# Optimization experiments

Measured on AMD Instinct MI355X. Metric: run time of the kernel, lower is better.

The kernel has to match this reference:

```python
import jax, jax.numpy as jnp
import numpy as np

N_NODES = 100000
N_EDGES = 1200000
MAX_ATOM_TYPE = 100
NUM_FEATURES = 92
GC_DIM = 64          # pre_layer_dim == gc_dim == CGConv channels
NUM_RBF = 32
NUM_GC_LAYERS = 4
CUTOFF_UPPER = 5.0
BN_EPS = 1e-5


def setup_inputs() -> dict:
    key = jax.random.key(0)
    ks = jax.random.split(key, 12)
    atom_types = jax.random.randint(ks[0], (N_NODES,), 0, MAX_ATOM_TYPE, dtype=jnp.int32)
    pos = jax.random.uniform(ks[1], (N_NODES, 3), dtype=jnp.float32) * 6.0  # box side 6 -> many dists < cutoff
    edge_index = jax.random.randint(ks[2], (2, N_EDGES), 0, N_NODES, dtype=jnp.int32)
    # parameters
    emb = jax.random.normal(ks[3], (MAX_ATOM_TYPE, NUM_FEATURES), dtype=jnp.float32)
    s = 1.0 / np.sqrt(NUM_FEATURES)
    pre_W = jax.random.uniform(ks[4], (NUM_FEATURES, GC_DIM), minval=-s, maxval=s, dtype=jnp.float32)
    pre_b = jnp.zeros((GC_DIM,), jnp.float32)
    zdim = 2 * GC_DIM + NUM_RBF  # [x_i, x_j, edge_attr]
    sz = 1.0 / np.sqrt(zdim)
    Wf = jax.random.uniform(ks[5], (NUM_GC_LAYERS, zdim, GC_DIM), minval=-sz, maxval=sz, dtype=jnp.float32)
    bf = jnp.zeros((NUM_GC_LAYERS, GC_DIM), jnp.float32)
    Ws = jax.random.uniform(ks[6], (NUM_GC_LAYERS, zdim, GC_DIM), minval=-sz, maxval=sz, dtype=jnp.float32)
    bs = jnp.zeros((NUM_GC_LAYERS, GC_DIM), jnp.float32)
    bn_gamma = jnp.ones((NUM_GC_LAYERS, GC_DIM), jnp.float32)
    bn_beta = jnp.zeros((NUM_GC_LAYERS, GC_DIM), jnp.float32)
    # ExpNormalSmearing (torchmd-net) init
    start = np.exp(-CUTOFF_UPPER)
    means = jnp.asarray(np.linspace(start, 1.0, NUM_RBF), jnp.float32)
    betas = jnp.full((NUM_RBF,), (2.0 / NUM_RBF * (1.0 - start)) ** -2, jnp.float32)
    return {"atom_types": atom_types, "pos": pos, "edge_index": edge_index,
            "emb": emb, "pre_W": pre_W, "pre_b": pre_b,
            "Wf": Wf, "bf": bf, "Ws": Ws, "bs": bs,
            "bn_gamma": bn_gamma, "bn_beta": bn_beta,
            "means": means, "betas": betas}


def _forward(atom_types, pos, edge_index, emb, pre_W, pre_b, Wf, bf, Ws, bs,
             bn_gamma, bn_beta, means, betas):
    src, dst = edge_index[0], edge_index[1]
    # distance (edge_vec = pos[src] - pos[dst])
    vec = pos[src] - pos[dst]                                  # [E,3]
    dist = jnp.sqrt(jnp.sum(vec * vec, axis=-1) + 1e-12)       # [E]
    # expnorm RBF with cosine cutoff (cutoff_lower = 0)
    cutoff = 0.5 * (jnp.cos(dist * (np.pi / CUTOFF_UPPER)) + 1.0) * (dist < CUTOFF_UPPER)
    alpha = 5.0 / CUTOFF_UPPER
    edge_attr = cutoff[:, None] * jnp.exp(
        -betas * (jnp.exp(-alpha * dist)[:, None] - means) ** 2)  # [E,NUM_RBF]
    # embedding + pre layer
    x = emb[atom_types]                                        # [N,F]
    x = jax.nn.relu(x @ pre_W + pre_b)                         # [N,C]
    # mean-aggregation degree (scatter-mean denominator)
    deg = jax.ops.segment_sum(jnp.ones_like(dist), dst, num_segments=N_NODES)
    inv_deg = jnp.where(deg > 0, 1.0 / jnp.maximum(deg, 1.0), 0.0)[:, None]
    for l in range(NUM_GC_LAYERS):
        # CGConv: z = [x_i, x_j, e]; out = x + mean_j(sigmoid(lin_f(z)) * softplus(lin_s(z)))
        z = jnp.concatenate([x[dst], x[src], edge_attr], axis=-1)   # [E, 2C+R]
        msg = jax.nn.sigmoid(z @ Wf[l] + bf[l]) * jax.nn.softplus(z @ Ws[l] + bs[l])
        agg = jax.ops.segment_sum(msg, dst, num_segments=N_NODES) * inv_deg
        x = x + agg
        # BatchNorm1d (batch statistics, biased var, as in torch training mode)
        mu = jnp.mean(x, axis=0)
        var = jnp.mean((x - mu) ** 2, axis=0)
        x = (x - mu) * jax.lax.rsqrt(var + BN_EPS) * bn_gamma[l] + bn_beta[l]
    return x


def reference(atom_types, pos, edge_index, emb, pre_W, pre_b, Wf, bf, Ws, bs,
              bn_gamma, bn_beta, means, betas):
    return _forward(atom_types, pos, edge_index, emb, pre_W, pre_b, Wf, bf, Ws, bs,
                    bn_gamma, bn_beta, means, betas)
```

## Files before the change

kernel.cpp:

```cpp
#include <hip/hip_runtime.h>
#include <math.h>

#define N_NODES 100000
#define N_EDGES 1200000
#define GC 64
#define RBF 32
#define NLAYERS 4
#define NF 92
#define NATOM 100
#define BN_EPS 1e-5f
#define TILE_GRID 2048
#define NWIN (N_EDGES / 16)
#define LOG2E 1.44269504f
#define LN2 0.69314718f

typedef _Float16 half8 __attribute__((ext_vector_type(8)));
typedef _Float16 half4 __attribute__((ext_vector_type(4)));
typedef _Float16 half2v __attribute__((ext_vector_type(2)));
typedef float f32x4 __attribute__((ext_vector_type(4)));
union U32H2 { unsigned int u; half2v h; };

__global__ __launch_bounds__(256) void deg_kernel(
    const int* __restrict__ ei, int* __restrict__ deg)
{
    int e = blockIdx.x * 256 + threadIdx.x;
    if (e >= N_EDGES) return;
    atomicAdd(&deg[ei[N_EDGES + e]], 1);
}

__global__ __launch_bounds__(256) void scan_a_kernel(const int* __restrict__ deg, int* __restrict__ bsums)
{
    __shared__ int sm[256];
    int tid = threadIdx.x;
    int i = blockIdx.x * 256 + tid;
    int v = (i < N_NODES) ? deg[i] : 0;
    sm[tid] = v;
    __syncthreads();
    for (int s = 128; s > 0; s >>= 1) {
        if (tid < s) sm[tid] += sm[tid + s];
        __syncthreads();
    }
    if (tid == 0) bsums[blockIdx.x] = sm[0];
}

__global__ __launch_bounds__(512) void scan_b_kernel(const int* __restrict__ bsums, int* __restrict__ boffs)
{
    __shared__ int sm[512];
    int tid = threadIdx.x;
    int v = (tid < 391) ? bsums[tid] : 0;
    sm[tid] = v;
    __syncthreads();
    for (int off = 1; off < 512; off <<= 1) {
        int t = (tid >= off) ? sm[tid - off] : 0;
        __syncthreads();
        sm[tid] += t;
        __syncthreads();
    }
    boffs[tid] = (tid == 0) ? 0 : sm[tid - 1];
}

__global__ __launch_bounds__(256) void scan_c_kernel(
    const int* __restrict__ deg, const int* __restrict__ boffs,
    int* __restrict__ row_st, float* __restrict__ inv_deg)
{
    __shared__ int sm[256];
    int tid = threadIdx.x;
    int i = blockIdx.x * 256 + tid;
    int v = (i < N_NODES) ? deg[i] : 0;
    sm[tid] = v;
    __syncthreads();
    for (int off = 1; off < 256; off <<= 1) {
        int t = (tid >= off) ? sm[tid - off] : 0;
        __syncthreads();
        sm[tid] += t;
        __syncthreads();
    }
    if (i <= N_NODES) row_st[i] = boffs[blockIdx.x] + sm[tid] - v;
    if (i < N_NODES) inv_deg[i] = (v > 0) ? (1.0f / (float)v) : 0.0f;
}

__global__ __launch_bounds__(256) void scatter_perm_kernel(
    const int* __restrict__ ei, const int* __restrict__ row_st,
    int* __restrict__ cursor, int2* __restrict__ csr_sd)
{
    int e = blockIdx.x * 256 + threadIdx.x;
    if (e >= N_EDGES) return;
    int s = ei[e];
    int d = ei[N_EDGES + e];
    int p = atomicAdd(&cursor[d], 1);
    csr_sd[row_st[d] + p] = make_int2(s, d);
}

__global__ __launch_bounds__(256) void split_kernel(
    const int2* __restrict__ csr_sd, int* __restrict__ csr_src, int* __restrict__ csr_dst)
{
    int i = blockIdx.x * 256 + threadIdx.x;
    if (i >= N_EDGES) return;
    int2 v = csr_sd[i];
    csr_src[i] = v.x;
    csr_dst[i] = v.y;
}

__global__ __launch_bounds__(256) void rbf_kernel(
    const int* __restrict__ csr_src, const int* __restrict__ csr_dst,
    const float* __restrict__ pos,
    const float* __restrict__ means, const float* __restrict__ betas,
    unsigned int* __restrict__ ea)
{
    int idx = blockIdx.x * 256 + threadIdx.x;
    if (idx >= N_EDGES) return;
    int s = csr_src[idx];
    int d = csr_dst[idx];
    float dx = pos[s * 3 + 0] - pos[d * 3 + 0];
    float dy = pos[s * 3 + 1] - pos[d * 3 + 1];
    float dz = pos[s * 3 + 2] - pos[d * 3 + 2];
    float dist = sqrtf(dx * dx + dy * dy + dz * dz + 1e-12f);

    float cut = 0.0f;
    if (dist < 5.0f) cut = 0.5f * (__cosf(dist * 0.6283185307179586f) + 1.0f);
    float ex = __expf(-dist);
    union { _Float16 h[32]; uint4 u[4]; } pk;
#pragma unroll
    for (int k = 0; k < 32; k++) {
        float v = ex - means[k];
        pk.h[k] = (_Float16)(cut * __expf(-betas[k] * v * v));
    }
    uint4* op = (uint4*)(ea + (size_t)idx * 16);
    op[0] = pk.u[0];
    op[1] = pk.u[1];
    op[2] = pk.u[2];
    op[3] = pk.u[3];
}

__global__ __launch_bounds__(256) void window_prep_kernel(
    const int* __restrict__ csr_dst, const float* __restrict__ inv_deg,
    unsigned char* __restrict__ seg8, int* __restrict__ wnode, _Float16* __restrict__ inv_e)
{
    int w = blockIdx.x * 256 + threadIdx.x;
    if (w >= NWIN) return;
    int base = w * 16;
    int prev = -1, s = -1;
    for (int k = 0; k < 16; k++) {
        int d = csr_dst[base + k];
        if (d != prev) { s++; prev = d; wnode[base + s] = d; }
        seg8[base + k] = (unsigned char)s;
        inv_e[base + k] = (_Float16)(inv_deg[d] * LN2);
    }
    for (int m = s + 1; m < 16; m++) wnode[base + m] = -1;
}

__global__ __launch_bounds__(256) void wcvt_kernel(
    const float* __restrict__ Wf, const float* __restrict__ Ws,
    _Float16* __restrict__ wf16, _Float16* __restrict__ ws16)
{
    int i = blockIdx.x * 256 + threadIdx.x;
    int l = i / (160 * GC);
    int r = i - l * 160 * GC;
    int k = r >> 6;
    int col = r & 63;
    size_t o = ((size_t)l * GC + col) * 160 + k;
    wf16[o] = (_Float16)(Wf[i] * LOG2E);
    ws16[o] = (_Float16)(Ws[i] * LOG2E);
}

__global__ __launch_bounds__(64) void atom_table_kernel(
    const float* __restrict__ emb, const float* __restrict__ pre_W,
    const float* __restrict__ pre_b, float* __restrict__ T)
{
    int a = blockIdx.x;
    int c = threadIdx.x;
    float acc = pre_b[c];
    for (int k = 0; k < NF; k++) acc = fmaf(emb[a * NF + k], pre_W[k * GC + c], acc);
    T[a * GC + c] = fmaxf(acc, 0.0f);
}

__global__ __launch_bounds__(256) void xinit_kernel(
    const int* __restrict__ atom_types, const float* __restrict__ T,
    float* __restrict__ x, _Float16* __restrict__ x16)
{
    int i = blockIdx.x * 256 + threadIdx.x;
    int n = i >> 4;
    int a = atom_types[n];
    float4 v = ((const float4*)T)[a * 16 + (i & 15)];
    ((float4*)x)[i] = v;
    half4 h = { (_Float16)v.x, (_Float16)v.y, (_Float16)v.z, (_Float16)v.w };
    ((half4*)x16)[i] = h;
}

static __device__ __forceinline__ void proj_mfma16(
    const _Float16* __restrict__ wf, const _Float16* __restrict__ ws,
    const float* __restrict__ bfv, const float* __restrict__ bsv,
    const half8 Bn[2], int cb, int node, unsigned int* __restrict__ P2u)
{
    const int lane = threadIdx.x & 63;
    const int quad = lane >> 4;
    const int r16 = lane & 15;
    f32x4 accf[2], accs[2];
#pragma unroll
    for (int sub = 0; sub < 2; sub++) {
        accf[sub] = (f32x4){0.f, 0.f, 0.f, 0.f};
        accs[sub] = (f32x4){0.f, 0.f, 0.f, 0.f};
    }
#pragma unroll
    for (int kt = 0; kt < 2; kt++) {
#pragma unroll
        for (int sub = 0; sub < 2; sub++) {
            int chan = cb + sub * 16 + r16;
            half8 a = *(const half8*)(wf + (size_t)chan * 160 + kt * 32 + quad * 8);
            half8 b = *(const half8*)(ws + (size_t)chan * 160 + kt * 32 + quad * 8);
            accf[sub] = __builtin_amdgcn_mfma_f32_16x16x32_f16(a, Bn[kt], accf[sub], 0, 0, 0);
            accs[sub] = __builtin_amdgcn_mfma_f32_16x16x32_f16(b, Bn[kt], accs[sub], 0, 0, 0);
        }
    }
#pragma unroll
    for (int sub = 0; sub < 2; sub++) {
        float4 bf4 = *(const float4*)(bfv + cb + sub * 16 + quad * 4);
        float4 bs4 = *(const float4*)(bsv + cb + sub * 16 + quad * 4);
        half8 h = { (_Float16)(accf[sub][0] + bf4.x * LOG2E), (_Float16)(accs[sub][0] + bs4.x * LOG2E),
                    (_Float16)(accf[sub][1] + bf4.y * LOG2E), (_Float16)(accs[sub][1] + bs4.y * LOG2E),
                    (_Float16)(accf[sub][2] + bf4.z * LOG2E), (_Float16)(accs[sub][2] + bs4.z * LOG2E),
                    (_Float16)(accf[sub][3] + bf4.w * LOG2E), (_Float16)(accs[sub][3] + bs4.w * LOG2E) };
        *(half8*)(P2u + (size_t)node * GC + cb + sub * 16 + quad * 4) = h;
    }
}

__global__ __launch_bounds__(256) void proj_kernel(
    const _Float16* __restrict__ x16,
    const _Float16* __restrict__ wf, const _Float16* __restrict__ ws,
    const float* __restrict__ bfv, const float* __restrict__ bsv,
    unsigned int* __restrict__ P2u)
{
    const int lane = threadIdx.x & 63;
    const int wid = threadIdx.x >> 6;
    const int quad = lane >> 4;
    const int r16 = lane & 15;
    const int wgid = blockIdx.x * 4 + wid;
    const int cb = (wgid & 1) * 32;
    const int nb = (wgid >> 1) * 16;
    half8 Bn[2];
    Bn[0] = *(const half8*)(x16 + (size_t)(nb + r16) * GC + quad * 8);
    Bn[1] = *(const half8*)(x16 + (size_t)(nb + r16) * GC + 32 + quad * 8);
    proj_mfma16(wf, ws, bfv, bsv, Bn, cb, nb + r16, P2u);
}

__global__ __launch_bounds__(256) void bnproj_kernel(
    const float* __restrict__ xn, const float* __restrict__ stats,
    const float* __restrict__ gamma, const float* __restrict__ beta,
    float* __restrict__ xout, _Float16* __restrict__ x16,
    const _Float16* __restrict__ wf, const _Float16* __restrict__ ws,
    const float* __restrict__ bfv, const float* __restrict__ bsv,
    unsigned int* __restrict__ P2u)
{
    __shared__ _Float16 lx[32 * 72];
    const int nb = blockIdx.x * 32;
    const float invN = 1.0f / (float)N_NODES;

#pragma unroll
    for (int rep = 0; rep < 2; rep++) {
        int g = rep * 256 + threadIdx.x;
        int gi = blockIdx.x * 512 + g;
        int node = g >> 4;
        int c4 = (g & 15) * 4;
        float4 v = ((const float4*)xn)[gi];
        float vv[4] = {v.x, v.y, v.z, v.w};
        float o[4];
#pragma unroll
        for (int t = 0; t < 4; t++) {
            int c = c4 + t;
            float mu = stats[c] * invN;
            float var = stats[64 + c] * invN - mu * mu;
            float sc = gamma[c] * rsqrtf(var + BN_EPS);
            o[t] = (vv[t] - mu) * sc + beta[c];
        }
        ((float4*)xout)[gi] = make_float4(o[0], o[1], o[2], o[3]);
        half4 h = { (_Float16)o[0], (_Float16)o[1], (_Float16)o[2], (_Float16)o[3] };
        ((half4*)x16)[gi] = h;
        *(half4*)(lx + node * 72 + c4) = h;
    }
    __syncthreads();

    const int lane = threadIdx.x & 63;
    const int wid = threadIdx.x >> 6;
    const int quad = lane >> 4;
    const int r16 = lane & 15;
    const int cb = (wid & 1) * 32;
    const int tn = (wid >> 1) * 16 + r16;
    half8 Bn[2];
    Bn[0] = *(const half8*)(lx + tn * 72 + quad * 8);
    Bn[1] = *(const half8*)(lx + tn * 72 + 32 + quad * 8);
    proj_mfma16(wf, ws, bfv, bsv, Bn, cb, nb + tn, P2u);
}

static __device__ __forceinline__ void compute_win(
    half8 S0, half8 S1, half8 E, int4 d4, int moff,
    const half8 (&WGF)[3][2], const half8 (&WGS)[3][2],
    int r16, int quad, int cb,
    const unsigned char* __restrict__ seg8, const int* __restrict__ wnode,
    const _Float16* __restrict__ inv_e, const unsigned int* __restrict__ P2u,
    float* __restrict__ x)
{
    unsigned int pv0, pv1, pv2, pv3, pv4, pv5, pv6, pv7;
    {
        const unsigned int* p0 = P2u + (size_t)d4.x * GC + cb + r16;
        const unsigned int* p1 = P2u + (size_t)d4.y * GC + cb + r16;
        const unsigned int* p2 = P2u + (size_t)d4.z * GC + cb + r16;
        const unsigned int* p3 = P2u + (size_t)d4.w * GC + cb + r16;
        pv0 = p0[0];  pv4 = p0[16];
        pv1 = p1[0];  pv5 = p1[16];
        pv2 = p2[0];  pv6 = p2[16];
        pv3 = p3[0];  pv7 = p3[16];
    }
    unsigned int segq = *(const unsigned int*)(seg8 + moff + quad * 4);
    int4 wn4 = *(const int4*)(wnode + moff + quad * 4);
    half4 inv4 = *(const half4*)(inv_e + moff + quad * 4);

    const f32x4 zf = (f32x4){0.0f, 0.0f, 0.0f, 0.0f};
    f32x4 accf[2], accs[2];
    __builtin_amdgcn_s_setprio(1);
#pragma unroll
    for (int ctl = 0; ctl < 2; ctl++) {
        accf[ctl] = __builtin_amdgcn_mfma_f32_16x16x32_f16(S0, WGF[0][ctl], zf, 0, 0, 0);
        accs[ctl] = __builtin_amdgcn_mfma_f32_16x16x32_f16(S0, WGS[0][ctl], zf, 0, 0, 0);
        accf[ctl] = __builtin_amdgcn_mfma_f32_16x16x32_f16(S1, WGF[1][ctl], accf[ctl], 0, 0, 0);
        accs[ctl] = __builtin_amdgcn_mfma_f32_16x16x32_f16(S1, WGS[1][ctl], accs[ctl], 0, 0, 0);
        accf[ctl] = __builtin_amdgcn_mfma_f32_16x16x32_f16(E,  WGF[2][ctl], accf[ctl], 0, 0, 0);
        accs[ctl] = __builtin_amdgcn_mfma_f32_16x16x32_f16(E,  WGS[2][ctl], accs[ctl], 0, 0, 0);
    }
    __builtin_amdgcn_s_setprio(0);

    unsigned int pvv[8] = {pv0, pv1, pv2, pv3, pv4, pv5, pv6, pv7};
    half4 msgh[2];
#pragma unroll
    for (int ctl = 0; ctl < 2; ctl++) {
#pragma unroll
        for (int rr = 0; rr < 4; rr++) {
            U32H2 t; t.u = pvv[ctl * 4 + rr];
            float af = accf[ctl][rr] + (float)t.h.x;
            float as = accs[ctl][rr] + (float)t.h.y;
            float sg = __builtin_amdgcn_rcpf(1.0f + __builtin_amdgcn_exp2f(-af));
            float sp = __builtin_amdgcn_logf(1.0f + __builtin_amdgcn_exp2f(as));
            msgh[ctl][rr] = (_Float16)(sg * sp);
        }
    }
    half4 am;
#pragma unroll
    for (int j = 0; j < 4; j++) {
        int sj = (segq >> (8 * j)) & 0xff;
        am[j] = (sj == r16) ? inv4[j] : (_Float16)0.0f;
    }
    int wa[4] = { wn4.x, wn4.y, wn4.z, wn4.w };
#pragma unroll
    for (int ctl = 0; ctl < 2; ctl++) {
        f32x4 red = __builtin_amdgcn_mfma_f32_16x16x16f16(am, msgh[ctl], zf, 0, 0, 0);
#pragma unroll
        for (int rr = 0; rr < 4; rr++) {
            int nd = wa[rr];
            if (nd >= 0) atomicAdd(&x[(size_t)nd * GC + cb + ctl * 16 + r16], red[rr]);
        }
    }
}

#define LOADSET(S0_, S1_, EE_, SRC_, WW_)                                            \
    S0_ = *(const half8*)(x16 + (size_t)(SRC_) * GC + quad * 8);                     \
    S1_ = *(const half8*)(x16 + (size_t)(SRC_) * GC + 32 + quad * 8);                \
    EE_ = *(const half8*)(ea + ((size_t)(WW_) * 16 + r16) * RBF + quad * 8);

__global__ __launch_bounds__(256, 4) void win_mfma_kernel(
    const _Float16* __restrict__ x16, const _Float16* __restrict__ ea,
    const int* __restrict__ csr_src, const int* __restrict__ csr_dst,
    const unsigned char* __restrict__ seg8, const int* __restrict__ wnode,
    const _Float16* __restrict__ inv_e, const unsigned int* __restrict__ P2u,
    const _Float16* __restrict__ wf16, const _Float16* __restrict__ ws16,
    float* __restrict__ x)
{
    const int lane = threadIdx.x & 63;
    const int wid = __builtin_amdgcn_readfirstlane(threadIdx.x >> 6);
    const int quad = lane >> 4;
    const int r16 = lane & 15;
    const int wgid = blockIdx.x * 4 + wid;
    const int cb = (wgid & 1) * 32;
    int w = wgid >> 1;
    const int NSEQ = TILE_GRID * 2;

    half8 WGF[3][2], WGS[3][2];
#pragma unroll
    for (int ctl = 0; ctl < 2; ctl++) {
        const _Float16* wfp = wf16 + (size_t)(cb + ctl * 16 + r16) * 160 + 64 + quad * 8;
        const _Float16* wsp = ws16 + (size_t)(cb + ctl * 16 + r16) * 160 + 64 + quad * 8;
#pragma unroll
        for (int kt = 0; kt < 3; kt++) {
            WGF[kt][ctl] = *(const half8*)(wfp + kt * 32);
            WGS[kt][ctl] = *(const half8*)(wsp + kt * 32);
        }
    }

    int sA = csr_src[w * 16 + r16];
    int4 d4A = *(const int4*)(csr_dst + w * 16 + quad * 4);
    half8 AS0, AS1, AE;
    LOADSET(AS0, AS1, AE, sA, w);
    int moffA = w * 16;

    int wB = w + NSEQ; if (wB >= NWIN) wB = NWIN - 1;
    int sB = csr_src[wB * 16 + r16];
    int4 d4B = *(const int4*)(csr_dst + wB * 16 + quad * 4);
    half8 BS0, BS1, BE;
    LOADSET(BS0, BS1, BE, sB, wB);
    int moffB = wB * 16;

    int wC = wB + NSEQ; if (wC >= NWIN) wC = NWIN - 1;
    int sC = csr_src[wC * 16 + r16];
    int4 d4C = *(const int4*)(csr_dst + wC * 16 + quad * 4);

    while (true) {
        compute_win(AS0, AS1, AE, d4A, moffA,
                    WGF, WGS, r16, quad, cb, seg8, wnode, inv_e, P2u, x);
        LOADSET(AS0, AS1, AE, sC, wC);
        d4A = d4C; moffA = wC * 16;
        wC += NSEQ; if (wC >= NWIN) wC = NWIN - 1;
        sC = csr_src[wC * 16 + r16];
        d4C = *(const int4*)(csr_dst + wC * 16 + quad * 4);
        w += NSEQ;
        if (w >= NWIN) break;

        compute_win(BS0, BS1, BE, d4B, moffB,
                    WGF, WGS, r16, quad, cb, seg8, wnode, inv_e, P2u, x);
        LOADSET(BS0, BS1, BE, sC, wC);
        d4B = d4C; moffB = wC * 16;
        wC += NSEQ; if (wC >= NWIN) wC = NWIN - 1;
        sC = csr_src[wC * 16 + r16];
        d4C = *(const int4*)(csr_dst + wC * 16 + quad * 4);
        w += NSEQ;
        if (w >= NWIN) break;
    }
}

__global__ __launch_bounds__(256) void stats_kernel(const float* __restrict__ x, float* __restrict__ stats)
{
    const int lane = threadIdx.x & 63;
    const int wid = threadIdx.x >> 6;
    int w = blockIdx.x * 4 + wid;
    float s1 = 0.0f, s2 = 0.0f;
    for (int n = w; n < N_NODES; n += 1024) {
        float v = x[(size_t)n * GC + lane];
        s1 += v;
        s2 = fmaf(v, v, s2);
    }
    __shared__ float rs1[4][64];
    __shared__ float rs2[4][64];
    rs1[wid][lane] = s1;
    rs2[wid][lane] = s2;
    __syncthreads();
    if (threadIdx.x < 64) {
        atomicAdd(&stats[lane], rs1[0][lane] + rs1[1][lane] + rs1[2][lane] + rs1[3][lane]);
    } else if (threadIdx.x < 128) {
        int c = threadIdx.x & 63;
        atomicAdd(&stats[64 + c], rs2[0][c] + rs2[1][c] + rs2[2][c] + rs2[3][c]);
    }
}

__global__ __launch_bounds__(256) void bn_kernel(
    const float* __restrict__ xn, const float* __restrict__ stats,
    const float* __restrict__ gamma, const float* __restrict__ beta,
    float* __restrict__ out)
{
    int i = blockIdx.x * 256 + threadIdx.x;
    int c4 = (i & 15) * 4;
    float4 v = ((const float4*)xn)[i];
    float vv[4] = {v.x, v.y, v.z, v.w};
    float o[4];
    const float invN = 1.0f / (float)N_NODES;
#pragma unroll
    for (int t = 0; t < 4; t++) {
        int c = c4 + t;
        float mu = stats[c] * invN;
        float var = stats[64 + c] * invN - mu * mu;
        float sc = gamma[c] * rsqrtf(var + BN_EPS);
        o[t] = (vv[t] - mu) * sc + beta[c];
    }
    ((float4*)out)[i] = make_float4(o[0], o[1], o[2], o[3]);
}

extern "C" void kernel_launch(void* const* d_in, const int* in_sizes, int n_in,
                              void* d_out, int out_size, void* d_ws, size_t ws_size,
                              hipStream_t stream)
{
    const int* atom_types = (const int*)d_in[0];
    const float* pos = (const float*)d_in[1];
    const int* edge_index = (const int*)d_in[2];
    const float* emb = (const float*)d_in[3];
    const float* pre_W = (const float*)d_in[4];
    const float* pre_b = (const float*)d_in[5];
    const float* Wf = (const float*)d_in[6];
    const float* bf = (const float*)d_in[7];
    const float* Ws = (const float*)d_in[8];
    const float* bs = (const float*)d_in[9];
    const float* gamma = (const float*)d_in[10];
    const float* beta = (const float*)d_in[11];
    const float* means = (const float*)d_in[12];
    const float* betas = (const float*)d_in[13];

    char* base = (char*)d_ws;
    char* p = base;
    auto alloc = [&](size_t bytes) -> char* {
        char* r = p;
        p += (bytes + 255) & ~(size_t)255;
        return r;
    };
    unsigned int* ea = (unsigned int*)alloc((size_t)N_EDGES * RBF * 2);
    float* x = (float*)alloc((size_t)N_NODES * GC * 4);
    _Float16* x16 = (_Float16*)alloc((size_t)N_NODES * GC * 2);
    unsigned int* P2u = (unsigned int*)alloc((size_t)N_NODES * GC * 4);
    int* csr_src = (int*)alloc((size_t)N_EDGES * 4);
    int* csr_dst = (int*)alloc((size_t)N_EDGES * 4);
    int* wnode = (int*)alloc((size_t)N_EDGES * 4);
    unsigned char* seg8 = (unsigned char*)alloc((size_t)N_EDGES);
    _Float16* inv_e = (_Float16*)alloc((size_t)N_EDGES * 2);
    _Float16* wf16 = (_Float16*)alloc((size_t)NLAYERS * GC * 160 * 2);
    _Float16* ws16 = (_Float16*)alloc((size_t)NLAYERS * GC * 160 * 2);
    int* row_st = (int*)alloc((size_t)(N_NODES + 1) * 4);
    float* inv_deg = (float*)alloc((size_t)N_NODES * 4);
    float* T = (float*)alloc((size_t)NATOM * GC * 4);
    int* bsums = (int*)alloc(512 * 4);
    int* boffs = (int*)alloc(512 * 4);
    const size_t ZR_INTS = (size_t)2 * N_NODES + 128 * NLAYERS + 64;
    char* zr = alloc(ZR_INTS * 4);
    int* deg = (int*)zr;
    int* cursor = deg + N_NODES;
    float* stats = (float*)(cursor + N_NODES);

    int2* csr_sd = (int2*)ea;

    if ((size_t)(p - base) > ws_size) return;

    (void)hipMemsetAsync(zr, 0, ZR_INTS * 4, stream);

    const int EG = (N_EDGES + 255) / 256;
    deg_kernel<<<EG, 256, 0, stream>>>(edge_index, deg);
    scan_a_kernel<<<391, 256, 0, stream>>>(deg, bsums);
    scan_b_kernel<<<1, 512, 0, stream>>>(bsums, boffs);
    scan_c_kernel<<<391, 256, 0, stream>>>(deg, boffs, row_st, inv_deg);
    scatter_perm_kernel<<<EG, 256, 0, stream>>>(edge_index, row_st, cursor, csr_sd);
    split_kernel<<<EG, 256, 0, stream>>>(csr_sd, csr_src, csr_dst);
    rbf_kernel<<<EG, 256, 0, stream>>>(csr_src, csr_dst, pos, means, betas, ea);
    window_prep_kernel<<<(NWIN + 255) / 256, 256, 0, stream>>>(csr_dst, inv_deg, seg8, wnode, inv_e);
    wcvt_kernel<<<(NLAYERS * 160 * GC) / 256, 256, 0, stream>>>(Wf, Ws, wf16, ws16);
    atom_table_kernel<<<NATOM, 64, 0, stream>>>(emb, pre_W, pre_b, T);
    xinit_kernel<<<N_NODES * 16 / 256, 256, 0, stream>>>(atom_types, T, x, x16);
    proj_kernel<<<N_NODES / 32, 256, 0, stream>>>(x16, wf16, ws16, bf, bs, P2u);

    for (int l = 0; l < NLAYERS; l++) {
        win_mfma_kernel<<<TILE_GRID, 256, 0, stream>>>(
            x16, (const _Float16*)ea, csr_src, csr_dst, seg8, wnode, inv_e, P2u,
            wf16 + (size_t)l * GC * 160, ws16 + (size_t)l * GC * 160, x);
        stats_kernel<<<256, 256, 0, stream>>>(x, stats + l * 128);
        if (l < NLAYERS - 1) {
            bnproj_kernel<<<N_NODES / 32, 256, 0, stream>>>(
                x, stats + l * 128, gamma + l * GC, beta + l * GC, x, x16,
                wf16 + (size_t)(l + 1) * GC * 160, ws16 + (size_t)(l + 1) * GC * 160,
                bf + (l + 1) * GC, bs + (l + 1) * GC, P2u);
        } else {
            bn_kernel<<<N_NODES * 16 / 256, 256, 0, stream>>>(
                x, stats + l * 128, gamma + l * GC, beta + l * GC, (float*)d_out);
        }
    }
}
```

Measured before the change: 891.2 us.

## Fuse edge preprocessing kernels, merge constant prep, retune occupancy and stats grid

Combines split, RBF and window-prep into one edge_post kernel that reads the sorted (src,dst) pairs once and builds the window segment data from shared memory. Weight conversion and the atom table go into a single launch, which cuts the number of kernel launches. csr_sd now gets its own buffer instead of aliasing ea, which costs extra workspace. The main kernel's launch bounds drop from 4 to 3 blocks per SM, and the stats kernel grid doubles to 512 blocks with the matching stride change.

```diff
diff --git a/kernel.cpp b/kernel.cpp
--- a/kernel.cpp
+++ b/kernel.cpp
@@ -91,87 +91,86 @@
     csr_sd[row_st[d] + p] = make_int2(s, d);
 }
 
-__global__ __launch_bounds__(256) void split_kernel(
-    const int2* __restrict__ csr_sd, int* __restrict__ csr_src, int* __restrict__ csr_dst)
-{
-    int i = blockIdx.x * 256 + threadIdx.x;
-    if (i >= N_EDGES) return;
-    int2 v = csr_sd[i];
-    csr_src[i] = v.x;
-    csr_dst[i] = v.y;
-}
-
-__global__ __launch_bounds__(256) void rbf_kernel(
-    const int* __restrict__ csr_src, const int* __restrict__ csr_dst,
-    const float* __restrict__ pos,
+__global__ __launch_bounds__(256) void edge_post_kernel(
+    const int2* __restrict__ csr_sd, const float* __restrict__ pos,
+    const float* __restrict__ inv_deg,
     const float* __restrict__ means, const float* __restrict__ betas,
-    unsigned int* __restrict__ ea)
-{
-    int idx = blockIdx.x * 256 + threadIdx.x;
-    if (idx >= N_EDGES) return;
-    int s = csr_src[idx];
-    int d = csr_dst[idx];
-    float dx = pos[s * 3 + 0] - pos[d * 3 + 0];
-    float dy = pos[s * 3 + 1] - pos[d * 3 + 1];
-    float dz = pos[s * 3 + 2] - pos[d * 3 + 2];
-    float dist = sqrtf(dx * dx + dy * dy + dz * dz + 1e-12f);
-
-    float cut = 0.0f;
-    if (dist < 5.0f) cut = 0.5f * (__cosf(dist * 0.6283185307179586f) + 1.0f);
-    float ex = __expf(-dist);
-    union { _Float16 h[32]; uint4 u[4]; } pk;
-#pragma unroll
-    for (int k = 0; k < 32; k++) {
-        float v = ex - means[k];
-        pk.h[k] = (_Float16)(cut * __expf(-betas[k] * v * v));
-    }
-    uint4* op = (uint4*)(ea + (size_t)idx * 16);
-    op[0] = pk.u[0];
-    op[1] = pk.u[1];
-    op[2] = pk.u[2];
-    op[3] = pk.u[3];
-}
-
-__global__ __launch_bounds__(256) void window_prep_kernel(
-    const int* __restrict__ csr_dst, const float* __restrict__ inv_deg,
-    unsigned char* __restrict__ seg8, int* __restrict__ wnode, _Float16* __restrict__ inv_e)
-{
-    int w = blockIdx.x * 256 + threadIdx.x;
-    if (w >= NWIN) return;
-    int base = w * 16;
-    int prev = -1, s = -1;
-    for (int k = 0; k < 16; k++) {
-        int d = csr_dst[base + k];
-        if (d != prev) { s++; prev = d; wnode[base + s] = d; }
-        seg8[base + k] = (unsigned char)s;
-        inv_e[base + k] = (_Float16)(inv_deg[d] * LN2);
-    }
-    for (int m = s + 1; m < 16; m++) wnode[base + m] = -1;
-}
-
-__global__ __launch_bounds__(256) void wcvt_kernel(
+    int* __restrict__ csr_src, int* __restrict__ csr_dst,
+    unsigned int* __restrict__ ea,
+    unsigned char* __restrict__ seg8, int* __restrict__ wnode,
+    _Float16* __restrict__ inv_e)
+{
+    __shared__ int sdst[256];
+    int t = blockIdx.x * 256 + threadIdx.x;
+    if (t < N_EDGES) {
+        int2 v = csr_sd[t];
+        int s = v.x, d = v.y;
+        csr_src[t] = s;
+        csr_dst[t] = d;
+        sdst[threadIdx.x] = d;
+        inv_e[t] = (_Float16)(inv_deg[d] * LN2);
+
+        float dx = pos[s * 3 + 0] - pos[d * 3 + 0];
+        float dy = pos[s * 3 + 1] - pos[d * 3 + 1];
+        float dz = pos[s * 3 + 2] - pos[d * 3 + 2];
+        float dist = sqrtf(dx * dx + dy * dy + dz * dz + 1e-12f);
+        float cut = 0.0f;
+        if (dist < 5.0f) cut = 0.5f * (__cosf(dist * 0.6283185307179586f) + 1.0f);
+        float ex = __expf(-dist);
+        union { _Float16 h[32]; uint4 u[4]; } pk;
+#pragma unroll
+        for (int k = 0; k < 32; k++) {
+            float vk = ex - means[k];
+            pk.h[k] = (_Float16)(cut * __expf(-betas[k] * vk * vk));
+        }
+        uint4* op = (uint4*)(ea + (size_t)t * 16);
+        op[0] = pk.u[0];
+        op[1] = pk.u[1];
+        op[2] = pk.u[2];
+        op[3] = pk.u[3];
+    }
+    __syncthreads();
+    if (threadIdx.x < 16) {
+        int w0 = blockIdx.x * 16 + threadIdx.x;
+        if ((size_t)w0 * 16 < N_EDGES) {
+            int lb = threadIdx.x * 16;
+            int gb = w0 * 16;
+            int prev = -1, sg = -1;
+            for (int k = 0; k < 16; k++) {
+                int dd = sdst[lb + k];
+                if (dd != prev) { sg++; prev = dd; wnode[gb + sg] = dd; }
+                seg8[gb + k] = (unsigned char)sg;
+            }
+            for (int m = sg + 1; m < 16; m++) wnode[gb + m] = -1;
+        }
+    }
+}
+
+__global__ __launch_bounds__(256) void prep_const_kernel(
     const float* __restrict__ Wf, const float* __restrict__ Ws,
-    _Float16* __restrict__ wf16, _Float16* __restrict__ ws16)
-{
-    int i = blockIdx.x * 256 + threadIdx.x;
-    int l = i / (160 * GC);
-    int r = i - l * 160 * GC;
-    int k = r >> 6;
-    int col = r & 63;
-    size_t o = ((size_t)l * GC + col) * 160 + k;
-    wf16[o] = (_Float16)(Wf[i] * LOG2E);
-    ws16[o] = (_Float16)(Ws[i] * LOG2E);
-}
-
-__global__ __launch_bounds__(64) void atom_table_kernel(
+    _Float16* __restrict__ wf16, _Float16* __restrict__ ws16,
     const float* __restrict__ emb, const float* __restrict__ pre_W,
     const float* __restrict__ pre_b, float* __restrict__ T)
 {
-    int a = blockIdx.x;
-    int c = threadIdx.x;
-    float acc = pre_b[c];
-    for (int k = 0; k < NF; k++) acc = fmaf(emb[a * NF + k], pre_W[k * GC + c], acc);
-    T[a * GC + c] = fmaxf(acc, 0.0f);
+    int b = blockIdx.x;
+    if (b < 160) {
+        int i = b * 256 + threadIdx.x;
+        int l = i / (160 * GC);
+        int r = i - l * 160 * GC;
+        int k = r >> 6;
+        int col = r & 63;
+        size_t o = ((size_t)l * GC + col) * 160 + k;
+        wf16[o] = (_Float16)(Wf[i] * LOG2E);
+        ws16[o] = (_Float16)(Ws[i] * LOG2E);
+    } else {
+        int a = (b - 160) * 4 + (threadIdx.x >> 6);
+        int c = threadIdx.x & 63;
+        if (a < NATOM) {
+            float acc = pre_b[c];
+            for (int k = 0; k < NF; k++) acc = fmaf(emb[a * NF + k], pre_W[k * GC + c], acc);
+            T[a * GC + c] = fmaxf(acc, 0.0f);
+        }
+    }
 }
 
 __global__ __launch_bounds__(256) void xinit_kernel(
@@ -365,7 +364,7 @@
     S1_ = *(const half8*)(x16 + (size_t)(SRC_) * GC + 32 + quad * 8);                \
     EE_ = *(const half8*)(ea + ((size_t)(WW_) * 16 + r16) * RBF + quad * 8);
 
-__global__ __launch_bounds__(256, 4) void win_mfma_kernel(
+__global__ __launch_bounds__(256, 3) void win_mfma_kernel(
     const _Float16* __restrict__ x16, const _Float16* __restrict__ ea,
     const int* __restrict__ csr_src, const int* __restrict__ csr_dst,
     const unsigned char* __restrict__ seg8, const int* __restrict__ wnode,
@@ -440,7 +439,7 @@
     const int wid = threadIdx.x >> 6;
     int w = blockIdx.x * 4 + wid;
     float s1 = 0.0f, s2 = 0.0f;
-    for (int n = w; n < N_NODES; n += 1024) {
+    for (int n = w; n < N_NODES; n += 2048) {
         float v = x[(size_t)n * GC + lane];
         s1 += v;
         s2 = fmaf(v, v, s2);
@@ -510,6 +509,7 @@
     float* x = (float*)alloc((size_t)N_NODES * GC * 4);
     _Float16* x16 = (_Float16*)alloc((size_t)N_NODES * GC * 2);
     unsigned int* P2u = (unsigned int*)alloc((size_t)N_NODES * GC * 4);
+    int2* csr_sd = (int2*)alloc((size_t)N_EDGES * 8);
     int* csr_src = (int*)alloc((size_t)N_EDGES * 4);
     int* csr_dst = (int*)alloc((size_t)N_EDGES * 4);
     int* wnode = (int*)alloc((size_t)N_EDGES * 4);
@@ -528,8 +528,6 @@
     int* cursor = deg + N_NODES;
     float* stats = (float*)(cursor + N_NODES);
 
-    int2* csr_sd = (int2*)ea;
-
     if ((size_t)(p - base) > ws_size) return;
 
     (void)hipMemsetAsync(zr, 0, ZR_INTS * 4, stream);
@@ -540,11 +538,9 @@
     scan_b_kernel<<<1, 512, 0, stream>>>(bsums, boffs);
     scan_c_kernel<<<391, 256, 0, stream>>>(deg, boffs, row_st, inv_deg);
     scatter_perm_kernel<<<EG, 256, 0, stream>>>(edge_index, row_st, cursor, csr_sd);
-    split_kernel<<<EG, 256, 0, stream>>>(csr_sd, csr_src, csr_dst);
-    rbf_kernel<<<EG, 256, 0, stream>>>(csr_src, csr_dst, pos, means, betas, ea);
-    window_prep_kernel<<<(NWIN + 255) / 256, 256, 0, stream>>>(csr_dst, inv_deg, seg8, wnode, inv_e);
-    wcvt_kernel<<<(NLAYERS * 160 * GC) / 256, 256, 0, stream>>>(Wf, Ws, wf16, ws16);
-    atom_table_kernel<<<NATOM, 64, 0, stream>>>(emb, pre_W, pre_b, T);
+    edge_post_kernel<<<EG, 256, 0, stream>>>(csr_sd, pos, inv_deg, means, betas,
+                                             csr_src, csr_dst, ea, seg8, wnode, inv_e);
+    prep_const_kernel<<<185, 256, 0, stream>>>(Wf, Ws, wf16, ws16, emb, pre_W, pre_b, T);
     xinit_kernel<<<N_NODES * 16 / 256, 256, 0, stream>>>(atom_types, T, x, x16);
     proj_kernel<<<N_NODES / 32, 256, 0, stream>>>(x16, wf16, ws16, bf, bs, P2u);
 
@@ -552,7 +548,7 @@
         win_mfma_kernel<<<TILE_GRID, 256, 0, stream>>>(
             x16, (const _Float16*)ea, csr_src, csr_dst, seg8, wnode, inv_e, P2u,
             wf16 + (size_t)l * GC * 160, ws16 + (size_t)l * GC * 160, x);
-        stats_kernel<<<256, 256, 0, stream>>>(x, stats + l * 128);
+        stats_kernel<<<512, 256, 0, stream>>>(x, stats + l * 128);
         if (l < NLAYERS - 1) {
             bnproj_kernel<<<N_NODES / 32, 256, 0, stream>>>(
                 x, stats + l * 128, gamma + l * GC, beta + l * GC, x, x16,
```

Result: faster. 816.4 us (-8.4%).
